# Kernel optimization log

Hardware: AMD Instinct MI355X
Metric: run time of the kernel (lower is better)

The kernel has to match this reference:

```python
import jax, jax.numpy as jnp
import numpy as np

NUM_TAGS = 96
PAD_IDX = 0
NEG = -10000.0


def setup_inputs() -> dict:
    key = jax.random.key(0)
    k1, k2, k3, k4, k5 = jax.random.split(key, 5)
    B, S, T = 128, 2048, NUM_TAGS
    emissions = jax.random.normal(k1, (B, S, T), dtype=jnp.float32)
    tags = jax.random.randint(k2, (B, S), 0, T, dtype=jnp.int64)
    mask = jnp.ones((B, S), dtype=jnp.float32)
    transitions = jax.random.normal(k3, (T, T), dtype=jnp.float32)
    transitions = transitions.at[PAD_IDX, :].set(NEG)
    transitions = transitions.at[:, PAD_IDX].set(NEG)
    transitions = transitions.at[PAD_IDX, PAD_IDX].set(0.0)
    start_transitions = jax.random.normal(k4, (T,), dtype=jnp.float32)
    start_transitions = start_transitions.at[PAD_IDX].set(NEG)
    end_transitions = jax.random.normal(k5, (T,), dtype=jnp.float32)
    return {"emissions": emissions, "tags": tags, "mask": mask,
            "transitions": transitions, "start_transitions": start_transitions,
            "end_transitions": end_transitions}


def _compute_score(emissions, tags, mask, transitions, start_transitions, end_transitions):
    # score of the gold path, fully vectorized over time
    score = start_transitions[tags[:, 0]]
    score = score + jnp.take_along_axis(emissions[:, 0], tags[:, 0:1], axis=1)[:, 0]
    trans = transitions[tags[:, :-1], tags[:, 1:]]                       # (B, S-1)
    emit = jnp.take_along_axis(emissions[:, 1:], tags[:, 1:, None], axis=2)[..., 0]
    score = score + jnp.sum((trans + emit) * mask[:, 1:], axis=1)
    last_pos = mask.astype(jnp.int32).sum(axis=1) - 1                    # (B,)
    last_tags = jnp.take_along_axis(tags, last_pos[:, None], axis=1)[:, 0]
    return score + end_transitions[last_tags]


def _log_partition(emissions, mask, transitions, start_transitions, end_transitions):
    # forward algorithm as a scan over time, alpha kept resident
    alpha0 = start_transitions[None, :] + emissions[:, 0]                # (B, T)
    em_rest = jnp.swapaxes(emissions[:, 1:], 0, 1)                       # (S-1, B, T)
    mk_rest = jnp.swapaxes(mask[:, 1:], 0, 1)                            # (S-1, B)

    def step(alpha, xs):
        emit_t, m_t = xs
        # (B, T_prev, T_next)
        nxt = jax.nn.logsumexp(alpha[:, :, None] + transitions[None] + emit_t[:, None, :], axis=1)
        m = m_t[:, None]
        return nxt * m + alpha * (1.0 - m), None

    alpha, _ = jax.lax.scan(step, alpha0, (em_rest, mk_rest))
    return jax.nn.logsumexp(alpha + end_transitions[None, :], axis=1)


def reference(emissions, tags, mask, transitions, start_transitions, end_transitions):
    mask = mask.astype(jnp.float32)
    log_num = _compute_score(emissions, tags, mask, transitions, start_transitions, end_transitions)
    log_den = _log_partition(emissions, mask, transitions, start_transitions, end_transitions)
    return jnp.mean(log_den - log_num)
```

## Files before the change

kernel.cpp:

```cpp
#include <hip/hip_runtime.h>
#include <hip/hip_bf16.h>
#include <math.h>

#define NTAG 96
#define NB   128
#define SLEN 2048
#define CPERB (SLEN * NTAG)
#define NCH  8
#define CHUNK 256

typedef __attribute__((ext_vector_type(8)))  short bf16x8;
typedef __attribute__((ext_vector_type(4)))  float f32x4;
typedef __attribute__((ext_vector_type(16))) float f32x16;
union U8 { unsigned int u[4]; bf16x8 v; };

__device__ __forceinline__ unsigned int pk2bf(float lo, float hi) {
    union { __hip_bfloat16 h; unsigned short u; } a, b;
    a.h = __float2bfloat16(lo);
    b.h = __float2bfloat16(hi);
    return (unsigned int)a.u | ((unsigned int)b.u << 16);
}

__device__ __forceinline__ float waveSum(float v) {
    #pragma unroll
    for (int o = 32; o > 0; o >>= 1) v += __shfl_xor(v, o);
    return v;
}

__global__ __launch_bounds__(256) void exp_pass(
    const float* __restrict__ x, float* __restrict__ y)
{
    size_t i = (size_t)blockIdx.x * 256 + threadIdx.x;
    f32x4 v = ((const f32x4*)x)[i];
    f32x4 o;
    o[0] = __expf(v[0]); o[1] = __expf(v[1]);
    o[2] = __expf(v[2]); o[3] = __expf(v[3]);
    ((f32x4*)y)[i] = o;
}

template <int IEXP>
__global__ __launch_bounds__(64, 2) void crf_chunk32(
    const float* __restrict__ srcE, const float* __restrict__ mask,
    const float* __restrict__ trans,
    float* __restrict__ P, float* __restrict__ Pls)
{
    const int tid = threadIdx.x;
    const int c = tid & 31;
    const int h = tid >> 5;

    const int k   = blockIdx.x;
    const int xcd = k & 7;
    const int seq = k >> 3;
    const int w2  = seq % 3;
    const int bcg = seq / 3;
    const int bc  = bcg * 8 + xcd;
    const int cch = bc & (NCH - 1);
    const int b   = bc >> 3;
    const int t0  = 1 + cch * CHUNK;
    const int t1  = min(SLEN, t0 + CHUNK);

    float tm = -1e30f;
    for (int q = tid; q < NTAG * NTAG; q += 64) tm = fmaxf(tm, trans[q]);
    #pragma unroll
    for (int o = 32; o > 0; o >>= 1) tm = fmaxf(tm, __shfl_xor(tm, o));
    const float tmax = tm;

    U8 Af[3][6];
    #pragma unroll
    for (int jt = 0; jt < 3; ++jt) {
        #pragma unroll
        for (int kt = 0; kt < 6; ++kt) {
            #pragma unroll
            for (int d = 0; d < 4; ++d) {
                int i0 = 16 * kt + 8 * h + 2 * d;
                Af[jt][kt].u[d] = pk2bf(
                    __expf(trans[i0 * NTAG + 32 * jt + c] - tmax),
                    __expf(trans[(i0 + 1) * NTAG + 32 * jt + c] - tmax));
            }
        }
    }

    float S[3][16];
    #pragma unroll
    for (int rt = 0; rt < 3; ++rt) {
        #pragma unroll
        for (int r = 0; r < 16; ++r)
            S[rt][r] = (32 * rt + (r & 3) + 8 * (r >> 2) + 4 * h == 32 * w2 + c)
                       ? 1.0f : 0.0f;
    }
    float ls = 0.0f;

#define RENORM() do { \
    float mx_ = S[0][0]; \
    _Pragma("unroll") \
    for (int rt_ = 0; rt_ < 3; ++rt_) { \
        _Pragma("unroll") \
        for (int r_ = 0; r_ < 16; ++r_) mx_ = fmaxf(mx_, S[rt_][r_]); \
    } \
    mx_ = fmaxf(mx_, __shfl_xor(mx_, 32)); \
    mx_ = fmaxf(mx_, 1e-30f); \
    float inv_ = 1.0f / mx_; \
    ls += __logf(mx_); \
    _Pragma("unroll") \
    for (int rt_ = 0; rt_ < 3; ++rt_) { \
        _Pragma("unroll") \
        for (int r_ = 0; r_ < 16; ++r_) S[rt_][r_] *= inv_; \
    } \
} while (0)

    U8 Bu[6];
#define MAKEB() do { \
    unsigned int pk_[3][8]; \
    _Pragma("unroll") \
    for (int rt_ = 0; rt_ < 3; ++rt_) { \
        _Pragma("unroll") \
        for (int p_ = 0; p_ < 8; ++p_) \
            pk_[rt_][p_] = pk2bf(S[rt_][2 * p_], S[rt_][2 * p_ + 1]); \
    } \
    _Pragma("unroll") \
    for (int kt_ = 0; kt_ < 6; ++kt_) { \
        const int rt_ = kt_ >> 1, q_ = 4 * (kt_ & 1); \
        unsigned int Y0_ = h ? pk_[rt_][q_]     : pk_[rt_][q_ + 2]; \
        unsigned int Y1_ = h ? pk_[rt_][q_ + 1] : pk_[rt_][q_ + 3]; \
        unsigned int r0_ = (unsigned int)__shfl_xor((int)Y0_, 32); \
        unsigned int r1_ = (unsigned int)__shfl_xor((int)Y1_, 32); \
        Bu[kt_].u[0] = h ? r0_ : pk_[rt_][q_]; \
        Bu[kt_].u[1] = h ? r1_ : pk_[rt_][q_ + 1]; \
        Bu[kt_].u[2] = h ? pk_[rt_][q_ + 2] : r0_; \
        Bu[kt_].u[3] = h ? pk_[rt_][q_ + 3] : r1_; \
    } \
} while (0)

    const float* eB  = srcE + (size_t)b * CPERB;
    const float* mkB = mask + (size_t)b * SLEN;
    const f32x16 z16 = {0.f,0.f,0.f,0.f,0.f,0.f,0.f,0.f,
                        0.f,0.f,0.f,0.f,0.f,0.f,0.f,0.f};

    f32x4 E[12];
#define LOADE(T) do { \
    const float* pE_ = eB + (size_t)(T) * NTAG + 4 * h; \
    _Pragma("unroll") \
    for (int rt_ = 0; rt_ < 3; ++rt_) { \
        _Pragma("unroll") \
        for (int q_ = 0; q_ < 4; ++q_) \
            E[rt_ * 4 + q_] = *(const f32x4*)(pE_ + 32 * rt_ + 8 * q_); \
    } \
} while (0)

#define STEPCORE(T) do { \
    LOADE(T); \
    f32x16 a0, a1, a2; \
    a0 = __builtin_amdgcn_mfma_f32_32x32x16_bf16(Af[0][0].v, Bu[0].v, z16, 0, 0, 0); \
    a1 = __builtin_amdgcn_mfma_f32_32x32x16_bf16(Af[1][0].v, Bu[0].v, z16, 0, 0, 0); \
    a2 = __builtin_amdgcn_mfma_f32_32x32x16_bf16(Af[2][0].v, Bu[0].v, z16, 0, 0, 0); \
    _Pragma("unroll") \
    for (int kt_ = 1; kt_ < 6; ++kt_) { \
        a0 = __builtin_amdgcn_mfma_f32_32x32x16_bf16(Af[0][kt_].v, Bu[kt_].v, a0, 0, 0, 0); \
        a1 = __builtin_amdgcn_mfma_f32_32x32x16_bf16(Af[1][kt_].v, Bu[kt_].v, a1, 0, 0, 0); \
        a2 = __builtin_amdgcn_mfma_f32_32x32x16_bf16(Af[2][kt_].v, Bu[kt_].v, a2, 0, 0, 0); \
    } \
    float mv_ = mkB[(T)]; \
    if (mv_ != 0.0f) { \
        _Pragma("unroll") \
        for (int r_ = 0; r_ < 16; ++r_) { \
            float e0_ = IEXP ? __expf(E[r_ >> 2][r_ & 3])     : E[r_ >> 2][r_ & 3]; \
            float e1_ = IEXP ? __expf(E[4 + (r_ >> 2)][r_ & 3]) : E[4 + (r_ >> 2)][r_ & 3]; \
            float e2_ = IEXP ? __expf(E[8 + (r_ >> 2)][r_ & 3]) : E[8 + (r_ >> 2)][r_ & 3]; \
            S[0][r_] = a0[r_] * e0_; \
            S[1][r_] = a1[r_] * e1_; \
            S[2][r_] = a2[r_] * e2_; \
        } \
        ls += tmax; \
    } \
} while (0)

#define STEP(T)   do { STEPCORE(T); MAKEB(); } while (0)
#define STEP_R(T) do { STEPCORE(T); RENORM(); MAKEB(); } while (0)

    MAKEB();

    const int nsteps = t1 - t0;
    const int nfull  = nsteps >> 3;
    int t = t0;
    #pragma unroll 1
    for (int blk = 0; blk < nfull; ++blk, t += 8) {
        STEP(t + 0); STEP(t + 1); STEP(t + 2); STEP(t + 3);
        STEP(t + 4); STEP(t + 5); STEP(t + 6); STEP_R(t + 7);
    }
    #pragma unroll 1
    while (t < t1) { STEP_R(t); ++t; }

    float* Pb = P + ((size_t)bc * NTAG + (32 * w2 + c)) * NTAG + 4 * h;
    #pragma unroll
    for (int rt = 0; rt < 3; ++rt) {
        #pragma unroll
        for (int q = 0; q < 4; ++q) {
            f32x4 v;
            v[0] = S[rt][4 * q + 0]; v[1] = S[rt][4 * q + 1];
            v[2] = S[rt][4 * q + 2]; v[3] = S[rt][4 * q + 3];
            *(f32x4*)(Pb + 32 * rt + 8 * q) = v;
        }
    }
    if (h == 0) Pls[(size_t)bc * NTAG + 32 * w2 + c] = ls;
#undef STEP
#undef STEP_R
#undef STEPCORE
#undef LOADE
#undef MAKEB
#undef RENORM
}

__global__ __launch_bounds__(128) void crf_fold(
    const float* __restrict__ em, const float* __restrict__ startT,
    const float* __restrict__ endT,
    const float* __restrict__ P, const float* __restrict__ Pls,
    float* __restrict__ den)
{
    __shared__ float aS[NTAG];
    __shared__ float sRed[2];
    const int b = blockIdx.x, tid = threadIdx.x;
    const bool act = tid < NTAG;

    float A = act ? (startT[tid] + em[(size_t)b * CPERB + tid]) : -1e30f;

    for (int c = 0; c < NCH; ++c) {
        const size_t bc = (size_t)b * NCH + c;
        float v = act ? (A + Pls[bc * NTAG + tid]) : -1e30f;
        float mv = v;
        #pragma unroll
        for (int o = 32; o > 0; o >>= 1) mv = fmaxf(mv, __shfl_xor(mv, o));
        if ((tid & 63) == 0) sRed[tid >> 6] = mv;
        __syncthreads();
        const float m = fmaxf(sRed[0], sRed[1]);
        __syncthreads();
        if (act) aS[tid] = __expf(v - m);
        __syncthreads();
        if (act) {
            const float* Pc = P + bc * (NTAG * NTAG) + tid;
            float dot = 0.f;
            #pragma unroll 8
            for (int i = 0; i < NTAG; ++i)
                dot = fmaf(aS[i], Pc[(size_t)i * NTAG], dot);
            A = m + __logf(dot);
        }
        __syncthreads();
    }

    float Afin = act ? (A + endT[tid]) : -1e30f;
    float mv = Afin;
    #pragma unroll
    for (int o = 32; o > 0; o >>= 1) mv = fmaxf(mv, __shfl_xor(mv, o));
    if ((tid & 63) == 0) sRed[tid >> 6] = mv;
    __syncthreads();
    const float m2 = fmaxf(sRed[0], sRed[1]);
    __syncthreads();
    float ex = act ? __expf(Afin - m2) : 0.f;
    ex = waveSum(ex);
    if ((tid & 63) == 0) sRed[tid >> 6] = ex;
    __syncthreads();
    if (tid == 0) den[b] = m2 + __logf(sRed[0] + sRed[1]);
}

__global__ __launch_bounds__(64, 1) void crf_forward_seq(
    const float* __restrict__ srcE, const float* __restrict__ srcM,
    const float* __restrict__ trans, const float* __restrict__ startT,
    const float* __restrict__ endT, float* __restrict__ den)
{
    __shared__ unsigned int lbuf[2][48 * 20];
    const int tid = threadIdx.x;
    const int g = tid >> 4;
    const int b16 = tid & 15;
    const int b = blockIdx.x * 16 + b16;

    float tm = -1e30f;
    for (int q = tid; q < NTAG * NTAG; q += 64) tm = fmaxf(tm, trans[q]);
    #pragma unroll
    for (int o = 32; o > 0; o >>= 1) tm = fmaxf(tm, __shfl_xor(tm, o));
    const float tmax = tm;

    bf16x8 Af[6][3];
    #pragma unroll
    for (int jt = 0; jt < 6; ++jt) {
        #pragma unroll
        for (int kf = 0; kf < 3; ++kf) {
            U8 u;
            #pragma unroll
            for (int d = 0; d < 4; ++d) {
                int i0 = 32 * kf + 8 * g + 2 * d;
                int j = 16 * jt + b16;
                u.u[d] = pk2bf(__expf(trans[i0 * NTAG + j] - tmax),
                               __expf(trans[(i0 + 1) * NTAG + j] - tmax));
            }
            Af[jt][kf] = u.v;
        }
    }

    float al[24];
    #pragma unroll
    for (int tile = 0; tile < 6; ++tile) {
        #pragma unroll
        for (int r = 0; r < 4; ++r) {
            int j = 16 * tile + 4 * g + r;
            al[tile * 4 + r] = __expf(startT[j]) * __expf(srcE[(size_t)b * CPERB + j]);
        }
    }
    float ls = 0.0f;

#define RENORM2() do { \
    float mx_ = al[0]; \
    _Pragma("unroll") \
    for (int k_ = 1; k_ < 24; ++k_) mx_ = fmaxf(mx_, al[k_]); \
    mx_ = fmaxf(mx_, __shfl_xor(mx_, 16)); \
    mx_ = fmaxf(mx_, __shfl_xor(mx_, 32)); \
    mx_ = fmaxf(mx_, 1e-30f); \
    float inv_ = 1.0f / mx_; \
    ls += __logf(mx_); \
    _Pragma("unroll") \
    for (int k_ = 0; k_ < 24; ++k_) al[k_] *= inv_; \
} while (0)

    U8 Bu[3];
#define MAKEB2(BUF) do { \
    _Pragma("unroll") \
    for (int t_ = 0; t_ < 6; ++t_) { \
        lbuf[BUF][(8 * t_ + 2 * g) * 20 + b16]     = pk2bf(al[4 * t_ + 0], al[4 * t_ + 1]); \
        lbuf[BUF][(8 * t_ + 2 * g + 1) * 20 + b16] = pk2bf(al[4 * t_ + 2], al[4 * t_ + 3]); \
    } \
    __syncthreads(); \
    _Pragma("unroll") \
    for (int kf_ = 0; kf_ < 3; ++kf_) { \
        _Pragma("unroll") \
        for (int d_ = 0; d_ < 4; ++d_) \
            Bu[kf_].u[d_] = lbuf[BUF][(16 * kf_ + 4 * g + d_) * 20 + b16]; \
    } \
} while (0)

    RENORM2();
    MAKEB2(0);
    const f32x4 zf4 = {0.f, 0.f, 0.f, 0.f};

    #pragma unroll 1
    for (int t = 1; t < SLEN; ++t) {
        f32x4 E[6];
        #pragma unroll
        for (int tl = 0; tl < 6; ++tl)
            E[tl] = *(const f32x4*)(srcE + (size_t)b * CPERB + (size_t)t * NTAG + 16 * tl + 4 * g);
        float mv = srcM[(size_t)b * SLEN + t];
        f32x4 acc[6];
        #pragma unroll
        for (int jt = 0; jt < 6; ++jt) {
            f32x4 a_ = __builtin_amdgcn_mfma_f32_16x16x32_bf16(Af[jt][0], Bu[0].v, zf4, 0, 0, 0);
            a_ = __builtin_amdgcn_mfma_f32_16x16x32_bf16(Af[jt][1], Bu[1].v, a_, 0, 0, 0);
            a_ = __builtin_amdgcn_mfma_f32_16x16x32_bf16(Af[jt][2], Bu[2].v, a_, 0, 0, 0);
            acc[jt] = a_;
        }
        bool km = (mv != 0.0f);
        #pragma unroll
        for (int tile = 0; tile < 6; ++tile) {
            #pragma unroll
            for (int r = 0; r < 4; ++r) {
                float nv = acc[tile][r] * __expf(E[tile][r]);
                al[tile * 4 + r] = km ? nv : al[tile * 4 + r];
            }
        }
        ls += km ? tmax : 0.0f;
        if ((t & 3) == 0) RENORM2();
        MAKEB2(t & 1);
        __syncthreads();
    }

    float s = 0.f;
    #pragma unroll
    for (int tile = 0; tile < 6; ++tile) {
        #pragma unroll
        for (int r = 0; r < 4; ++r) {
            int j = 16 * tile + 4 * g + r;
            s += al[tile * 4 + r] * __expf(endT[j]);
        }
    }
    s += __shfl_xor(s, 16);
    s += __shfl_xor(s, 32);
    if (tid < 16) den[b] = ls + __logf(s);
#undef MAKEB2
#undef RENORM2
}

__global__ __launch_bounds__(256) void crf_score(
    const float* __restrict__ em, const int* __restrict__ tags,
    const float* __restrict__ mask, const float* __restrict__ trans,
    const float* __restrict__ startT, const float* __restrict__ endT,
    float* __restrict__ num)
{
    __shared__ float sS[4], sM[4];
    const int b = blockIdx.x, tid = threadIdx.x;
    const float* emB = em + (size_t)b * CPERB;
    const int* tgB = tags + (size_t)b * SLEN;
    const float* mkB = mask + (size_t)b * SLEN;

    float part = 0.f, mcnt = 0.f;
    for (int t = tid; t < SLEN; t += 256) {
        float mt = mkB[t];
        mcnt += mt;
        if (t >= 1) {
            int tp = tgB[t - 1], tc = tgB[t];
            part += (trans[tp * NTAG + tc] + emB[(size_t)t * NTAG + tc]) * mt;
        }
    }
    part = waveSum(part);
    mcnt = waveSum(mcnt);
    if ((tid & 63) == 0) { sS[tid >> 6] = part; sM[tid >> 6] = mcnt; }
    __syncthreads();
    if (tid == 0) {
        float tot = sS[0] + sS[1] + sS[2] + sS[3];
        int last = (int)(sM[0] + sM[1] + sM[2] + sM[3]) - 1;
        int t0 = tgB[0];
        num[b] = tot + startT[t0] + emB[t0] + endT[tgB[last]];
    }
}

__global__ __launch_bounds__(128) void crf_final(
    const float* __restrict__ den, const float* __restrict__ num,
    float* __restrict__ out)
{
    __shared__ float s2[2];
    const int tid = threadIdx.x;
    float v = den[tid] - num[tid];
    v = waveSum(v);
    if ((tid & 63) == 0) s2[tid >> 6] = v;
    __syncthreads();
    if (tid == 0) out[0] = (s2[0] + s2[1]) * (1.0f / NB);
}

extern "C" void kernel_launch(void* const* d_in, const int* in_sizes, int n_in,
                              void* d_out, int out_size, void* d_ws, size_t ws_size,
                              hipStream_t stream) {
    const float* em     = (const float*)d_in[0];
    const int*   tags   = (const int*)d_in[1];
    const float* mask   = (const float*)d_in[2];
    const float* trans  = (const float*)d_in[3];
    const float* startT = (const float*)d_in[4];
    const float* endT   = (const float*)d_in[5];
    float* out = (float*)d_out;
    float* num = (float*)d_ws;
    float* den = num + NB;

    const size_t szP   = (size_t)NB * NCH * NTAG * NTAG;
    const size_t szPls = (size_t)NB * NCH * NTAG;
    float* P    = (float*)((char*)d_ws + 4096);
    float* Pls  = P + szP;
    float* eexp = Pls + szPls;
    const size_t need_mid  = 4096 + (szP + szPls) * 4;
    const size_t need_full = need_mid + (size_t)NB * CPERB * 4;

    crf_score<<<NB, 256, 0, stream>>>(em, tags, mask, trans, startT, endT, num);
    if (ws_size >= need_full) {
        exp_pass<<<(NB * CPERB) / (256 * 4), 256, 0, stream>>>(em, eexp);
        crf_chunk32<0><<<3 * NB * NCH, 64, 0, stream>>>(eexp, mask, trans, P, Pls);
        crf_fold<<<NB, 128, 0, stream>>>(em, startT, endT, P, Pls, den);
    } else if (ws_size >= need_mid) {
        crf_chunk32<1><<<3 * NB * NCH, 64, 0, stream>>>(em, mask, trans, P, Pls);
        crf_fold<<<NB, 128, 0, stream>>>(em, startT, endT, P, Pls, den);
    } else {
        crf_forward_seq<<<NB / 16, 64, 0, stream>>>(em, mask, trans, startT, endT, den);
    }
    crf_final<<<1, 128, 0, stream>>>(den, num, out);
}
```

Measured before the change: 697.1 us.

## Store exp'd emissions as bf16 and split sequence into 16 chunks

The precomputed exp(emissions) buffer is written in bf16 instead of fp32, which halves the write traffic of the exp pass and the read traffic of the chunk kernel. The chunk kernel unpacks the bf16 values with bit shifts. The sequence is also split into 16 chunks of 128 steps instead of 8 of 256, doubling the number of independent blocks so the serial recurrence per block is shorter. In exchange the fold kernel has twice as many partial matrices to combine, and emission factors lose precision.

```diff
diff --git a/kernel.cpp b/kernel.cpp
--- a/kernel.cpp
+++ b/kernel.cpp
@@ -6,8 +6,8 @@
 #define NB   128
 #define SLEN 2048
 #define CPERB (SLEN * NTAG)
-#define NCH  8
-#define CHUNK 256
+#define NCH  16
+#define CHUNK 128
 
 typedef __attribute__((ext_vector_type(8)))  short bf16x8;
 typedef __attribute__((ext_vector_type(4)))  float f32x4;
@@ -20,6 +20,12 @@
     b.h = __float2bfloat16(hi);
     return (unsigned int)a.u | ((unsigned int)b.u << 16);
 }
+__device__ __forceinline__ float bf16lo(unsigned int u) {
+    union { unsigned int i; float f; } x; x.i = u << 16; return x.f;
+}
+__device__ __forceinline__ float bf16hi(unsigned int u) {
+    union { unsigned int i; float f; } x; x.i = u & 0xffff0000u; return x.f;
+}
 
 __device__ __forceinline__ float waveSum(float v) {
     #pragma unroll
@@ -27,20 +33,20 @@
     return v;
 }
 
-__global__ __launch_bounds__(256) void exp_pass(
-    const float* __restrict__ x, float* __restrict__ y)
+__global__ __launch_bounds__(256) void exp_pass_bf16(
+    const float* __restrict__ x, unsigned int* __restrict__ y)
 {
     size_t i = (size_t)blockIdx.x * 256 + threadIdx.x;
     f32x4 v = ((const f32x4*)x)[i];
-    f32x4 o;
-    o[0] = __expf(v[0]); o[1] = __expf(v[1]);
-    o[2] = __expf(v[2]); o[3] = __expf(v[3]);
-    ((f32x4*)y)[i] = o;
+    uint2 o;
+    o.x = pk2bf(__expf(v[0]), __expf(v[1]));
+    o.y = pk2bf(__expf(v[2]), __expf(v[3]));
+    ((uint2*)y)[i] = o;
 }
 
 template <int IEXP>
 __global__ __launch_bounds__(64, 2) void crf_chunk32(
-    const float* __restrict__ srcE, const float* __restrict__ mask,
+    const void* __restrict__ srcE, const float* __restrict__ mask,
     const float* __restrict__ trans,
     float* __restrict__ P, float* __restrict__ Pls)
 {
@@ -55,7 +61,7 @@
     const int bcg = seq / 3;
     const int bc  = bcg * 8 + xcd;
     const int cch = bc & (NCH - 1);
-    const int b   = bc >> 3;
+    const int b   = bc >> 4;
     const int t0  = 1 + cch * CHUNK;
     const int t1  = min(SLEN, t0 + CHUNK);
 
@@ -131,19 +137,32 @@
     } \
 } while (0)
 
-    const float* eB  = srcE + (size_t)b * CPERB;
     const float* mkB = mask + (size_t)b * SLEN;
     const f32x16 z16 = {0.f,0.f,0.f,0.f,0.f,0.f,0.f,0.f,
                         0.f,0.f,0.f,0.f,0.f,0.f,0.f,0.f};
 
-    f32x4 E[12];
+    const unsigned short* eH = (const unsigned short*)srcE + (size_t)b * CPERB;
+    const float*          eF = (const float*)srcE + (size_t)b * CPERB;
+
+    uint2 E2[12];
+    f32x4 E4[12];
 #define LOADE(T) do { \
-    const float* pE_ = eB + (size_t)(T) * NTAG + 4 * h; \
-    _Pragma("unroll") \
-    for (int rt_ = 0; rt_ < 3; ++rt_) { \
-        _Pragma("unroll") \
-        for (int q_ = 0; q_ < 4; ++q_) \
-            E[rt_ * 4 + q_] = *(const f32x4*)(pE_ + 32 * rt_ + 8 * q_); \
+    if (IEXP) { \
+        const float* pE_ = eF + (size_t)(T) * NTAG + 4 * h; \
+        _Pragma("unroll") \
+        for (int rt_ = 0; rt_ < 3; ++rt_) { \
+            _Pragma("unroll") \
+            for (int q_ = 0; q_ < 4; ++q_) \
+                E4[rt_ * 4 + q_] = *(const f32x4*)(pE_ + 32 * rt_ + 8 * q_); \
+        } \
+    } else { \
+        const unsigned short* pH_ = eH + (size_t)(T) * NTAG + 4 * h; \
+        _Pragma("unroll") \
+        for (int rt_ = 0; rt_ < 3; ++rt_) { \
+            _Pragma("unroll") \
+            for (int q_ = 0; q_ < 4; ++q_) \
+                E2[rt_ * 4 + q_] = *(const uint2*)(pH_ + 32 * rt_ + 8 * q_); \
+        } \
     } \
 } while (0)
 
@@ -162,13 +181,26 @@
     float mv_ = mkB[(T)]; \
     if (mv_ != 0.0f) { \
         _Pragma("unroll") \
-        for (int r_ = 0; r_ < 16; ++r_) { \
-            float e0_ = IEXP ? __expf(E[r_ >> 2][r_ & 3])     : E[r_ >> 2][r_ & 3]; \
-            float e1_ = IEXP ? __expf(E[4 + (r_ >> 2)][r_ & 3]) : E[4 + (r_ >> 2)][r_ & 3]; \
-            float e2_ = IEXP ? __expf(E[8 + (r_ >> 2)][r_ & 3]) : E[8 + (r_ >> 2)][r_ & 3]; \
-            S[0][r_] = a0[r_] * e0_; \
-            S[1][r_] = a1[r_] * e1_; \
-            S[2][r_] = a2[r_] * e2_; \
+        for (int rt_ = 0; rt_ < 3; ++rt_) { \
+            f32x16 ac_ = (rt_ == 0) ? a0 : ((rt_ == 1) ? a1 : a2); \
+            _Pragma("unroll") \
+            for (int q_ = 0; q_ < 4; ++q_) { \
+                float e0_, e1_, e2_, e3_; \
+                if (IEXP) { \
+                    e0_ = __expf(E4[rt_ * 4 + q_][0]); \
+                    e1_ = __expf(E4[rt_ * 4 + q_][1]); \
+                    e2_ = __expf(E4[rt_ * 4 + q_][2]); \
+                    e3_ = __expf(E4[rt_ * 4 + q_][3]); \
+                } else { \
+                    uint2 u_ = E2[rt_ * 4 + q_]; \
+                    e0_ = bf16lo(u_.x); e1_ = bf16hi(u_.x); \
+                    e2_ = bf16lo(u_.y); e3_ = bf16hi(u_.y); \
+                } \
+                S[rt_][4 * q_ + 0] = ac_[4 * q_ + 0] * e0_; \
+                S[rt_][4 * q_ + 1] = ac_[4 * q_ + 1] * e1_; \
+                S[rt_][4 * q_ + 2] = ac_[4 * q_ + 2] * e2_; \
+                S[rt_][4 * q_ + 3] = ac_[4 * q_ + 3] * e3_; \
+            } \
         } \
         ls += tmax; \
     } \
@@ -448,14 +480,14 @@
     const size_t szPls = (size_t)NB * NCH * NTAG;
     float* P    = (float*)((char*)d_ws + 4096);
     float* Pls  = P + szP;
-    float* eexp = Pls + szPls;
+    unsigned int* eexpH = (unsigned int*)(Pls + szPls);
     const size_t need_mid  = 4096 + (szP + szPls) * 4;
-    const size_t need_full = need_mid + (size_t)NB * CPERB * 4;
+    const size_t need_full = need_mid + (size_t)NB * CPERB * 2;
 
     crf_score<<<NB, 256, 0, stream>>>(em, tags, mask, trans, startT, endT, num);
     if (ws_size >= need_full) {
-        exp_pass<<<(NB * CPERB) / (256 * 4), 256, 0, stream>>>(em, eexp);
-        crf_chunk32<0><<<3 * NB * NCH, 64, 0, stream>>>(eexp, mask, trans, P, Pls);
+        exp_pass_bf16<<<(NB * CPERB) / (256 * 4), 256, 0, stream>>>(em, eexpH);
+        crf_chunk32<0><<<3 * NB * NCH, 64, 0, stream>>>(eexpH, mask, trans, P, Pls);
         crf_fold<<<NB, 128, 0, stream>>>(em, startT, endT, P, Pls, den);
     } else if (ws_size >= need_mid) {
         crf_chunk32<1><<<3 * NB * NCH, 64, 0, stream>>>(em, mask, trans, P, Pls);
```

Measured after the change: 732.9 us. 1.05x slower.
